# Optimization experiments

Measured on AMD Instinct MI355X. Metric: run time of the kernel, lower is better.

The kernel has to match this reference:

```python
import jax, jax.numpy as jnp
import numpy as np

NUM_HEADS = 12

def setup_inputs() -> dict:
    key = jax.random.key(0)
    k1, k2, k3 = jax.random.split(key, 3)
    dim = 768
    x = jax.random.normal(k1, (1, 64, 64, dim), dtype=jnp.float32)
    qkv_w = jax.random.normal(k2, (3 * dim, dim), dtype=jnp.float32) * (dim ** -0.5)
    qkv_b = jnp.zeros((3 * dim,), dtype=jnp.float32)
    proj_w = jax.random.normal(k3, (dim, dim), dtype=jnp.float32) * (dim ** -0.5)
    proj_b = jnp.zeros((dim,), dtype=jnp.float32)
    return {"x": x, "qkv_w": qkv_w, "qkv_b": qkv_b, "proj_w": proj_w, "proj_b": proj_b}

def reference(x, qkv_w, qkv_b, proj_w, proj_b):
    B, H, W, C = x.shape
    N = H * W
    nh = NUM_HEADS
    # qkv projection: [B,H,W,3C] -> [B,N,3,nh,hd]
    qkv = jnp.einsum('bhwc,dc->bhwd', x, qkv_w) + qkv_b
    qkv = qkv.reshape(B, N, 3, nh, -1)
    q, k, v = qkv[:, :, 0], qkv[:, :, 1], qkv[:, :, 2]  # [B,N,nh,hd]
    q = q.transpose(0, 2, 1, 3)  # [B,nh,N,hd]
    k = k.transpose(0, 2, 1, 3)
    v = v.transpose(0, 2, 1, 3)
    hd = q.shape[-1]
    scale = hd ** -0.5
    scores = jnp.einsum('bhnd,bhmd->bhnm', q, k) * scale  # [B,nh,N,N]
    attn = jax.nn.softmax(scores.astype(jnp.float32), axis=-1).astype(q.dtype)
    attn = jax.lax.stop_gradient(attn)
    out = jnp.einsum('bhnm,bhmd->bhnd', attn, v)  # [B,nh,N,hd]
    out = out.transpose(0, 2, 1, 3).reshape(B, H, W, -1)
    out = jnp.einsum('bhwc,dc->bhwd', out, proj_w) + proj_b
    return out
```

## Files before the change

### kernel.cpp

```cpp
#include <hip/hip_runtime.h>

typedef short short8 __attribute__((ext_vector_type(8)));
typedef short short2v __attribute__((ext_vector_type(2)));
typedef float f32x4 __attribute__((ext_vector_type(4)));
typedef float f32x16 __attribute__((ext_vector_type(16)));
typedef unsigned short ushort4v __attribute__((ext_vector_type(4)));
typedef unsigned int u32;
typedef unsigned int u32x4 __attribute__((ext_vector_type(4)));

__device__ __forceinline__ unsigned short f2b(float f) {
  unsigned u = __builtin_bit_cast(unsigned, f);
  u = u + 0x7FFFu + ((u >> 16) & 1u);
  return (unsigned short)(u >> 16);
}

__device__ __forceinline__ void bar_plain() {
  __builtin_amdgcn_sched_barrier(0);
  asm volatile("" ::: "memory");
  __builtin_amdgcn_s_barrier();
  asm volatile("" ::: "memory");
  __builtin_amdgcn_sched_barrier(0);
}
__device__ __forceinline__ void bar_lgkm() {
  __builtin_amdgcn_sched_barrier(0);
  asm volatile("s_waitcnt lgkmcnt(0)" ::: "memory");
  __builtin_amdgcn_s_barrier();
  asm volatile("" ::: "memory");
  __builtin_amdgcn_sched_barrier(0);
}

__global__ void f2bf3_kernel(const float* __restrict__ a, unsigned short* __restrict__ oa, int na,
                             const float* __restrict__ b, unsigned short* __restrict__ ob, int nb,
                             const float* __restrict__ c, unsigned short* __restrict__ oc, int nc) {
  int i = blockIdx.x * blockDim.x + threadIdx.x;
  const float* in; unsigned short* out;
  if (i < na)           { in = a; out = oa; }
  else if (i < na + nb) { i -= na; in = b; out = ob; }
  else if (i < na + nb + nc) { i -= na + nb; in = c; out = oc; }
  else return;
  float4 v = reinterpret_cast<const float4*>(in)[i];
  ushort4v o;
  o.x = f2b(v.x); o.y = f2b(v.y); o.z = f2b(v.z); o.w = f2b(v.w);
  reinterpret_cast<ushort4v*>(out)[i] = o;
}

__device__ __forceinline__ void store_out(float* C, int idx, float v) { C[idx] = v; }
__device__ __forceinline__ void store_out(short* C, int idx, float v) { C[idx] = (short)f2b(v); }

template <typename OutT>
__global__ __launch_bounds__(256, 2)
void gemm_bt_kernel(const short* __restrict__ A, const short* __restrict__ B,
                    const float* __restrict__ bias, OutT* __restrict__ C,
                    int M, int N, int K, int qcols, float qscale)
{
  __shared__ __align__(16) short lds_a[128][72];
  __shared__ __align__(16) short lds_b[128][72];

  const int tid  = threadIdx.x;
  const int lane = tid & 63;
  const int wave = tid >> 6;
  const int wm   = wave >> 1;
  const int wn   = wave & 1;
  const int r16  = lane & 15;
  const int q4   = lane >> 4;
  const int bm   = blockIdx.x;
  const int bn   = blockIdx.y;

  f32x4 zero = {0.f, 0.f, 0.f, 0.f};
  f32x4 acc[4][4];
#pragma unroll
  for (int i = 0; i < 4; ++i)
#pragma unroll
    for (int j = 0; j < 4; ++j) acc[i][j] = zero;

  const int srow = tid >> 3;
  const int scol = (tid & 7) * 8;
  const short* Ab = A + (bm * 128 + srow) * K + scol;
  const short* Bb = B + (bn * 128 + srow) * K + scol;

  short8 ar[4], br[4];
#pragma unroll
  for (int i = 0; i < 4; ++i) {
    ar[i] = *reinterpret_cast<const short8*>(Ab + i * 32 * K);
    br[i] = *reinterpret_cast<const short8*>(Bb + i * 32 * K);
  }

  const int nk = K >> 6;
  for (int kt = 0; kt < nk; ++kt) {
#pragma unroll
    for (int i = 0; i < 4; ++i) {
      *reinterpret_cast<short8*>(&lds_a[srow + i * 32][scol]) = ar[i];
      *reinterpret_cast<short8*>(&lds_b[srow + i * 32][scol]) = br[i];
    }
    bar_lgkm();
    if (kt + 1 < nk) {
      const short* An = Ab + (kt + 1) * 64;
      const short* Bn = Bb + (kt + 1) * 64;
#pragma unroll
      for (int i = 0; i < 4; ++i) {
        ar[i] = *reinterpret_cast<const short8*>(An + i * 32 * K);
        br[i] = *reinterpret_cast<const short8*>(Bn + i * 32 * K);
      }
    }
#pragma unroll
    for (int kk = 0; kk < 2; ++kk) {
      short8 af[4], bf[4];
#pragma unroll
      for (int mi = 0; mi < 4; ++mi)
        af[mi] = *reinterpret_cast<const short8*>(&lds_a[wm * 64 + mi * 16 + r16][kk * 32 + q4 * 8]);
#pragma unroll
      for (int ni = 0; ni < 4; ++ni)
        bf[ni] = *reinterpret_cast<const short8*>(&lds_b[wn * 64 + ni * 16 + r16][kk * 32 + q4 * 8]);
#pragma unroll
      for (int mi = 0; mi < 4; ++mi)
#pragma unroll
        for (int ni = 0; ni < 4; ++ni)
          acc[mi][ni] = __builtin_amdgcn_mfma_f32_16x16x32_bf16(af[mi], bf[ni], acc[mi][ni], 0, 0, 0);
    }
    bar_plain();
  }

#pragma unroll
  for (int mi = 0; mi < 4; ++mi) {
    const int row0 = bm * 128 + wm * 64 + mi * 16 + q4 * 4;
#pragma unroll
    for (int ni = 0; ni < 4; ++ni) {
      const int col = bn * 128 + wn * 64 + ni * 16 + r16;
      const float bz = bias[col];
      const float sc = (col < qcols) ? qscale : 1.f;
#pragma unroll
      for (int j = 0; j < 4; ++j)
        store_out(C, (row0 + j) * N + col, (acc[mi][ni][j] + bz) * sc);
    }
  }
}

__global__ __launch_bounds__(256, 3)
void attn_kernel(const short* __restrict__ QKV, short* __restrict__ Ao)
{
  constexpr int C3 = 2304;
  __shared__ __align__(16) short k_lds[2][64][64];
  __shared__ __align__(16) short v_lds[2][2][64][64];

  const int tid  = threadIdx.x;
  const int lane = tid & 63;
  const int wave = tid >> 6;
  const int sp   = wave >> 1;
  const int qh   = wave & 1;
  const int l31  = lane & 31;
  const int hi   = lane >> 5;
  const int swz  = l31 & 7;
  const int h    = blockIdx.y;
  const int qt   = blockIdx.x;

  const short* Qp = QKV + h * 64;

  const int qrow = qt * 64 + qh * 32 + l31;
  short8 qf[4];
#pragma unroll
  for (int ks = 0; ks < 4; ++ks)
    qf[ks] = *reinterpret_cast<const short8*>(Qp + qrow * C3 + ks * 16 + hi * 8);

  const int t2 = tid & 127;
  const int kr = t2 >> 3;
  const int kc = t2 & 7;
  const int kswz = 8 * (kc ^ (kr & 7));

  const short* Kt = QKV + 768  + h * 64 + (size_t)(sp * 2048 + kr)     * C3 + kc * 8;
  const short* Vt = QKV + 1536 + h * 64 + (size_t)(sp * 2048 + 2 * kr) * C3 + kc * 8;

  short8 ka[4], va[4];
  auto LOADT = [&]() {
#pragma unroll
    for (int j = 0; j < 4; ++j)
      ka[j] = *reinterpret_cast<const short8*>(Kt + j * 16 * C3);
    va[0] = *reinterpret_cast<const short8*>(Vt);
    va[1] = *reinterpret_cast<const short8*>(Vt + C3);
    va[2] = *reinterpret_cast<const short8*>(Vt + 32 * C3);
    va[3] = *reinterpret_cast<const short8*>(Vt + 33 * C3);
    Kt += 64 * C3; Vt += 64 * C3;
  };

  const int vb3_0 = (2 * kr) >> 3, vko = (2 * kr) & 7;

  short* const vw0 = &v_lds[sp][0][0][0];
  short* const vw1 = &v_lds[sp][1][0][0];
  short* vwr = vw0;
  short* vww = vw1;

  auto WRITET = [&](short* vb) {
#pragma unroll
    for (int j = 0; j < 4; ++j)
      *reinterpret_cast<short8*>(&k_lds[sp][kr + 16 * j][kswz]) = ka[j];
#pragma unroll
    for (int p = 0; p < 2; ++p) {
      const int b3 = vb3_0 + 4 * p;
#pragma unroll
      for (int i = 0; i < 8; ++i) {
        short2v pr; pr.x = va[2 * p][i]; pr.y = va[2 * p + 1][i];
        *reinterpret_cast<short2v*>(vb + (kc * 8 + i) * 64 + 8 * (b3 ^ kc ^ i) + vko) = pr;
      }
    }
  };

  const f32x16 ZEROv = {};
  const short ONE_BF = (short)0x3F80;
  const short8 ONESv = {ONE_BF, ONE_BF, ONE_BF, ONE_BF, ONE_BF, ONE_BF, ONE_BF, ONE_BF};

  f32x16 o0 = {}, o1 = {}, acc_l = {};

  LOADT();
  WRITET(vw0);
  LOADT();
  bar_lgkm();

  for (int kt = 0; kt < 32; ++kt) {
    f32x16 s0, s1;
    {
      const short* kb0 = &k_lds[sp][l31][0];
      const short* kb1 = &k_lds[sp][l31 + 32][0];
      __builtin_amdgcn_s_setprio(1);
#pragma unroll
      for (int ks = 0; ks < 4; ++ks) {
        const int off = 8 * (((ks << 1) | hi) ^ swz);
        short8 kf0 = *reinterpret_cast<const short8*>(kb0 + off);
        short8 kf1 = *reinterpret_cast<const short8*>(kb1 + off);
        s0 = __builtin_amdgcn_mfma_f32_32x32x16_bf16(kf0, qf[ks], ks ? s0 : ZEROv, 0, 0, 0);
        s1 = __builtin_amdgcn_mfma_f32_32x32x16_bf16(kf1, qf[ks], ks ? s1 : ZEROv, 0, 0, 0);
      }
      __builtin_amdgcn_s_setprio(0);
    }
    bar_plain();

    if (kt != 31) {
      WRITET(vww);
      if (kt != 30) LOADT();
    }

#pragma unroll
    for (int i = 0; i < 16; ++i) {
      s0[i] = __builtin_amdgcn_exp2f(s0[i]);
      s1[i] = __builtin_amdgcn_exp2f(s1[i]);
    }

    u32 pkv[4][4];
#pragma unroll
    for (int t = 0; t < 4; ++t) {
      asm("v_cvt_pk_bf16_f32 %0, %1, %2" : "=v"(pkv[0][t]) : "v"(s0[2 * t]),     "v"(s0[2 * t + 1]));
      asm("v_cvt_pk_bf16_f32 %0, %1, %2" : "=v"(pkv[1][t]) : "v"(s0[8 + 2 * t]), "v"(s0[8 + 2 * t + 1]));
      asm("v_cvt_pk_bf16_f32 %0, %1, %2" : "=v"(pkv[2][t]) : "v"(s1[2 * t]),     "v"(s1[2 * t + 1]));
      asm("v_cvt_pk_bf16_f32 %0, %1, %2" : "=v"(pkv[3][t]) : "v"(s1[8 + 2 * t]), "v"(s1[8 + 2 * t + 1]));
    }
#pragma unroll
    for (int ks = 0; ks < 4; ++ks) {
      asm("v_permlane32_swap_b32 %0, %1" : "+v"(pkv[ks][0]), "+v"(pkv[ks][2]));
      asm("v_permlane32_swap_b32 %0, %1" : "+v"(pkv[ks][1]), "+v"(pkv[ks][3]));
    }
    short8 pa[4];
#pragma unroll
    for (int ks = 0; ks < 4; ++ks) {
      u32x4 tmp = {pkv[ks][0], pkv[ks][1], pkv[ks][2], pkv[ks][3]};
      pa[ks] = __builtin_bit_cast(short8, tmp);
    }

#pragma unroll
    for (int ks = 0; ks < 4; ++ks)
      acc_l = __builtin_amdgcn_mfma_f32_32x32x16_bf16(pa[ks], ONESv, acc_l, 0, 0, 0);

    {
      const short* vb0 = vwr + l31 * 64;
      const short* vb1 = vwr + (l31 + 32) * 64;
      const int rsw = (l31 >> 3) ^ (l31 & 7);
      __builtin_amdgcn_s_setprio(1);
#pragma unroll
      for (int ks = 0; ks < 4; ++ks) {
        const int c = ((ks << 1) | hi) ^ rsw;
        short8 vf0 = *reinterpret_cast<const short8*>(vb0 + 8 * c);
        short8 vf1 = *reinterpret_cast<const short8*>(vb1 + 8 * (c ^ 4));
        o0 = __builtin_amdgcn_mfma_f32_32x32x16_bf16(pa[ks], vf0, o0, 0, 0, 0);
        o1 = __builtin_amdgcn_mfma_f32_32x32x16_bf16(pa[ks], vf1, o1, 0, 0, 0);
      }
      __builtin_amdgcn_s_setprio(0);
    }

    { short* t = vwr; vwr = vww; vww = t; }
    bar_lgkm();
  }

  float* o_sh = (float*)&k_lds[0][0][0];
  float* l_sh = (float*)&v_lds[0][0][0][0];

  __syncthreads();
  if (sp == 1) {
#pragma unroll
    for (int r = 0; r < 16; ++r) {
      const int q = (r & 3) + 8 * (r >> 2) + 4 * hi;
      const int row = qh * 32 + q;
      o_sh[row * 64 + l31]      = o0[r];
      o_sh[row * 64 + 32 + l31] = o1[r];
    }
    if (l31 == 0) {
#pragma unroll
      for (int r = 0; r < 16; ++r) {
        const int q = (r & 3) + 8 * (r >> 2) + 4 * hi;
        l_sh[qh * 32 + q] = acc_l[r];
      }
    }
  }
  __syncthreads();
  if (sp == 0) {
#pragma unroll
    for (int r = 0; r < 16; ++r) {
      const int q = (r & 3) + 8 * (r >> 2) + 4 * hi;
      const int row = qh * 32 + q;
      const float lt = 1.f / (acc_l[r] + l_sh[row]);
      const int grow = qt * 64 + row;
      float a0 = (o0[r] + o_sh[row * 64 + l31]) * lt;
      float a1 = (o1[r] + o_sh[row * 64 + 32 + l31]) * lt;
      Ao[grow * 768 + h * 64 + l31]      = (short)f2b(a0);
      Ao[grow * 768 + h * 64 + 32 + l31] = (short)f2b(a1);
    }
  }
}

extern "C" void kernel_launch(void* const* d_in, const int* in_sizes, int n_in,
                              void* d_out, int out_size, void* d_ws, size_t ws_size,
                              hipStream_t stream)
{
  const float* x      = (const float*)d_in[0];
  const float* qkv_w  = (const float*)d_in[1];
  const float* qkv_b  = (const float*)d_in[2];
  const float* proj_w = (const float*)d_in[3];
  const float* proj_b = (const float*)d_in[4];
  float* out = (float*)d_out;

  char* ws = (char*)d_ws;
  short* xb  = (short*)(ws + 0);
  short* wq  = (short*)(ws + 6291456);
  short* wp  = (short*)(ws + 9830400);
  short* qkv = (short*)(ws + 11010048);
  short* ao  = (short*)(ws + 29884416);

  const float sscale = 0.125f * 1.44269504088896340736f;

  f2bf3_kernel<<<5376, 256, 0, stream>>>(x, (unsigned short*)xb, 786432,
                                         qkv_w, (unsigned short*)wq, 442368,
                                         proj_w, (unsigned short*)wp, 147456);

  gemm_bt_kernel<short><<<dim3(32, 18), 256, 0, stream>>>(xb, wq, qkv_b, qkv, 4096, 2304, 768, 768, sscale);
  attn_kernel<<<dim3(64, 12), 256, 0, stream>>>(qkv, ao);
  gemm_bt_kernel<float><<<dim3(32, 6), 256, 0, stream>>>(ao, wp, proj_b, out, 4096, 768, 768, 0, 1.f);
}
```

Baseline: 128.5 us.

## Give each attention wave private K/V LDS tiles and drop block barriers

The attention kernel now gives each wave its own K and V LDS region, which it loads and transposes itself. This replaces the shared double-buffered tiles and the two block-wide barriers per iteration with per-wave lgkmcnt waits. The aim is to remove inter-wave synchronisation stalls, at the cost of duplicate global/L2 loads of K/V across the paired query waves, a larger LDS footprint and more registers per wave. Launch bounds also change: the GEMM goes to 3 blocks per SM and attention to 2.

```diff
diff --git a/kernel.cpp b/kernel.cpp
--- a/kernel.cpp
+++ b/kernel.cpp
@@ -1,7 +1,7 @@
 #include <hip/hip_runtime.h>
 
 typedef short short8 __attribute__((ext_vector_type(8)));
-typedef short short2v __attribute__((ext_vector_type(2)));
+typedef short short4v __attribute__((ext_vector_type(4)));
 typedef float f32x4 __attribute__((ext_vector_type(4)));
 typedef float f32x16 __attribute__((ext_vector_type(16)));
 typedef unsigned short ushort4v __attribute__((ext_vector_type(4)));
@@ -48,7 +48,7 @@
 __device__ __forceinline__ void store_out(short* C, int idx, float v) { C[idx] = (short)f2b(v); }
 
 template <typename OutT>
-__global__ __launch_bounds__(256, 2)
+__global__ __launch_bounds__(256, 3)
 void gemm_bt_kernel(const short* __restrict__ A, const short* __restrict__ B,
                     const float* __restrict__ bias, OutT* __restrict__ C,
                     int M, int N, int K, int qcols, float qscale)
@@ -135,12 +135,11 @@
   }
 }
 
-__global__ __launch_bounds__(256, 3)
+__global__ __launch_bounds__(256, 2)
 void attn_kernel(const short* __restrict__ QKV, short* __restrict__ Ao)
 {
   constexpr int C3 = 2304;
-  __shared__ __align__(16) short k_lds[2][64][64];
-  __shared__ __align__(16) short v_lds[2][2][64][64];
+  __shared__ __align__(16) short kv[4][2][64][64];
 
   const int tid  = threadIdx.x;
   const int lane = tid & 63;
@@ -153,72 +152,74 @@
   const int h    = blockIdx.y;
   const int qt   = blockIdx.x;
 
-  const short* Qp = QKV + h * 64;
-
   const int qrow = qt * 64 + qh * 32 + l31;
   short8 qf[4];
 #pragma unroll
   for (int ks = 0; ks < 4; ++ks)
-    qf[ks] = *reinterpret_cast<const short8*>(Qp + qrow * C3 + ks * 16 + hi * 8);
-
-  const int t2 = tid & 127;
-  const int kr = t2 >> 3;
-  const int kc = t2 & 7;
-  const int kswz = 8 * (kc ^ (kr & 7));
+    qf[ks] = *reinterpret_cast<const short8*>(QKV + h * 64 + qrow * C3 + ks * 16 + hi * 8);
+
+  const int kr = lane >> 3;
+  const int kc = lane & 7;
+  short* const kp = &kv[wave][0][0][0];
+  short* const vp = &kv[wave][1][0][0];
+  const int kswz = 8 * (kc ^ kr);
 
   const short* Kt = QKV + 768  + h * 64 + (size_t)(sp * 2048 + kr)     * C3 + kc * 8;
-  const short* Vt = QKV + 1536 + h * 64 + (size_t)(sp * 2048 + 2 * kr) * C3 + kc * 8;
-
-  short8 ka[4], va[4];
+  const short* Vt = QKV + 1536 + h * 64 + (size_t)(sp * 2048 + 4 * kr) * C3 + kc * 8;
+
+  short8 ka[8], va[8];
   auto LOADT = [&]() {
 #pragma unroll
-    for (int j = 0; j < 4; ++j)
-      ka[j] = *reinterpret_cast<const short8*>(Kt + j * 16 * C3);
-    va[0] = *reinterpret_cast<const short8*>(Vt);
-    va[1] = *reinterpret_cast<const short8*>(Vt + C3);
-    va[2] = *reinterpret_cast<const short8*>(Vt + 32 * C3);
-    va[3] = *reinterpret_cast<const short8*>(Vt + 33 * C3);
+    for (int j = 0; j < 8; ++j)
+      ka[j] = *reinterpret_cast<const short8*>(Kt + j * 8 * C3);
+#pragma unroll
+    for (int j = 0; j < 4; ++j) {
+      va[j]     = *reinterpret_cast<const short8*>(Vt + j * C3);
+      va[4 + j] = *reinterpret_cast<const short8*>(Vt + (32 + j) * C3);
+    }
     Kt += 64 * C3; Vt += 64 * C3;
   };
 
-  const int vb3_0 = (2 * kr) >> 3, vko = (2 * kr) & 7;
-
-  short* const vw0 = &v_lds[sp][0][0][0];
-  short* const vw1 = &v_lds[sp][1][0][0];
-  short* vwr = vw0;
-  short* vww = vw1;
-
-  auto WRITET = [&](short* vb) {
-#pragma unroll
-    for (int j = 0; j < 4; ++j)
-      *reinterpret_cast<short8*>(&k_lds[sp][kr + 16 * j][kswz]) = ka[j];
-#pragma unroll
-    for (int p = 0; p < 2; ++p) {
-      const int b3 = vb3_0 + 4 * p;
-#pragma unroll
-      for (int i = 0; i < 8; ++i) {
-        short2v pr; pr.x = va[2 * p][i]; pr.y = va[2 * p + 1][i];
-        *reinterpret_cast<short2v*>(vb + (kc * 8 + i) * 64 + 8 * (b3 ^ kc ^ i) + vko) = pr;
-      }
+  const int vco = 4 * (kr & 1);
+  const int vch = kr >> 1;
+  auto WRITET = [&]() {
+#pragma unroll
+    for (int j = 0; j < 8; ++j)
+      *reinterpret_cast<short8*>(kp + (kr + 8 * j) * 64 + kswz) = ka[j];
+#pragma unroll
+    for (int i = 0; i < 8; ++i) {
+      short4v p0 = {va[0][i], va[1][i], va[2][i], va[3][i]};
+      short4v p1 = {va[4][i], va[5][i], va[6][i], va[7][i]};
+      const int base = (kc * 8 + i) * 64 + vco;
+      const int c0 = vch ^ kc ^ i;
+      *reinterpret_cast<short4v*>(vp + base + 8 * c0)       = p0;
+      *reinterpret_cast<short4v*>(vp + base + 8 * (c0 ^ 4)) = p1;
     }
   };
 
   const f32x16 ZEROv = {};
   const short ONE_BF = (short)0x3F80;
   const short8 ONESv = {ONE_BF, ONE_BF, ONE_BF, ONE_BF, ONE_BF, ONE_BF, ONE_BF, ONE_BF};
+  const int rsw = (l31 >> 3) ^ (l31 & 7);
 
   f32x16 o0 = {}, o1 = {}, acc_l = {};
 
   LOADT();
-  WRITET(vw0);
-  LOADT();
-  bar_lgkm();
 
   for (int kt = 0; kt < 32; ++kt) {
+    asm volatile("s_waitcnt lgkmcnt(0)" ::: "memory");
+    __builtin_amdgcn_sched_barrier(0);
+
+    WRITET();
+    if (kt != 31) LOADT();
+
+    asm volatile("s_waitcnt lgkmcnt(0)" ::: "memory");
+    __builtin_amdgcn_sched_barrier(0);
+
     f32x16 s0, s1;
     {
-      const short* kb0 = &k_lds[sp][l31][0];
-      const short* kb1 = &k_lds[sp][l31 + 32][0];
+      const short* kb0 = kp + l31 * 64;
+      const short* kb1 = kp + (l31 + 32) * 64;
       __builtin_amdgcn_s_setprio(1);
 #pragma unroll
       for (int ks = 0; ks < 4; ++ks) {
@@ -230,12 +231,6 @@
       }
       __builtin_amdgcn_s_setprio(0);
     }
-    bar_plain();
-
-    if (kt != 31) {
-      WRITET(vww);
-      if (kt != 30) LOADT();
-    }
 
 #pragma unroll
     for (int i = 0; i < 16; ++i) {
@@ -268,9 +263,8 @@
       acc_l = __builtin_amdgcn_mfma_f32_32x32x16_bf16(pa[ks], ONESv, acc_l, 0, 0, 0);
 
     {
-      const short* vb0 = vwr + l31 * 64;
-      const short* vb1 = vwr + (l31 + 32) * 64;
-      const int rsw = (l31 >> 3) ^ (l31 & 7);
+      const short* vb0 = vp + l31 * 64;
+      const short* vb1 = vp + (l31 + 32) * 64;
       __builtin_amdgcn_s_setprio(1);
 #pragma unroll
       for (int ks = 0; ks < 4; ++ks) {
@@ -282,15 +276,13 @@
       }
       __builtin_amdgcn_s_setprio(0);
     }
-
-    { short* t = vwr; vwr = vww; vww = t; }
-    bar_lgkm();
-  }
-
-  float* o_sh = (float*)&k_lds[0][0][0];
-  float* l_sh = (float*)&v_lds[0][0][0][0];
+  }
 
   __syncthreads();
+
+  float* o_sh = (float*)&kv[0][0][0][0];
+  float* l_sh = (float*)&kv[1][0][0][0];
+
   if (sp == 1) {
 #pragma unroll
     for (int r = 0; r < 16; ++r) {
```

Result: slower. 144.6 us (+12.6%).

## Drop split-KV in attention: one 128-thread block walks all keys

Applied to the files above, without the earlier changes.

The attention kernel no longer splits the key range across two wave pairs. Each block now has two waves that loop over all 64 key tiles and normalize directly, which removes the cross-wave reduction through shared memory and its two syncthreads, and halves LDS use per block. The cost is half the waves per block and a sequential loop twice as long, so per-CU latency hiding now depends on fitting more resident blocks. The GEMM launch bound is also raised to three blocks per SIMD, which limits register allocation.

```diff
diff --git a/kernel.cpp b/kernel.cpp
--- a/kernel.cpp
+++ b/kernel.cpp
@@ -48,7 +48,7 @@
 __device__ __forceinline__ void store_out(short* C, int idx, float v) { C[idx] = (short)f2b(v); }
 
 template <typename OutT>
-__global__ __launch_bounds__(256, 2)
+__global__ __launch_bounds__(256, 3)
 void gemm_bt_kernel(const short* __restrict__ A, const short* __restrict__ B,
                     const float* __restrict__ bias, OutT* __restrict__ C,
                     int M, int N, int K, int qcols, float qscale)
@@ -135,39 +135,34 @@
   }
 }
 
-__global__ __launch_bounds__(256, 3)
+__global__ __launch_bounds__(128, 3)
 void attn_kernel(const short* __restrict__ QKV, short* __restrict__ Ao)
 {
   constexpr int C3 = 2304;
-  __shared__ __align__(16) short k_lds[2][64][64];
-  __shared__ __align__(16) short v_lds[2][2][64][64];
+  __shared__ __align__(16) short k_lds[64][64];
+  __shared__ __align__(16) short v_lds[2][64][64];
 
   const int tid  = threadIdx.x;
   const int lane = tid & 63;
   const int wave = tid >> 6;
-  const int sp   = wave >> 1;
-  const int qh   = wave & 1;
   const int l31  = lane & 31;
   const int hi   = lane >> 5;
   const int swz  = l31 & 7;
   const int h    = blockIdx.y;
   const int qt   = blockIdx.x;
 
-  const short* Qp = QKV + h * 64;
-
-  const int qrow = qt * 64 + qh * 32 + l31;
+  const int qrow = qt * 64 + wave * 32 + l31;
   short8 qf[4];
 #pragma unroll
   for (int ks = 0; ks < 4; ++ks)
-    qf[ks] = *reinterpret_cast<const short8*>(Qp + qrow * C3 + ks * 16 + hi * 8);
-
-  const int t2 = tid & 127;
-  const int kr = t2 >> 3;
-  const int kc = t2 & 7;
+    qf[ks] = *reinterpret_cast<const short8*>(QKV + h * 64 + qrow * C3 + ks * 16 + hi * 8);
+
+  const int kr = tid >> 3;
+  const int kc = tid & 7;
   const int kswz = 8 * (kc ^ (kr & 7));
 
-  const short* Kt = QKV + 768  + h * 64 + (size_t)(sp * 2048 + kr)     * C3 + kc * 8;
-  const short* Vt = QKV + 1536 + h * 64 + (size_t)(sp * 2048 + 2 * kr) * C3 + kc * 8;
+  const short* Kt = QKV + 768  + h * 64 + (size_t)kr       * C3 + kc * 8;
+  const short* Vt = QKV + 1536 + h * 64 + (size_t)(2 * kr) * C3 + kc * 8;
 
   short8 ka[4], va[4];
   auto LOADT = [&]() {
@@ -183,15 +178,15 @@
 
   const int vb3_0 = (2 * kr) >> 3, vko = (2 * kr) & 7;
 
-  short* const vw0 = &v_lds[sp][0][0][0];
-  short* const vw1 = &v_lds[sp][1][0][0];
+  short* const vw0 = &v_lds[0][0][0];
+  short* const vw1 = &v_lds[1][0][0];
   short* vwr = vw0;
   short* vww = vw1;
 
   auto WRITET = [&](short* vb) {
 #pragma unroll
     for (int j = 0; j < 4; ++j)
-      *reinterpret_cast<short8*>(&k_lds[sp][kr + 16 * j][kswz]) = ka[j];
+      *reinterpret_cast<short8*>(&k_lds[kr + 16 * j][kswz]) = ka[j];
 #pragma unroll
     for (int p = 0; p < 2; ++p) {
       const int b3 = vb3_0 + 4 * p;
@@ -214,11 +209,11 @@
   LOADT();
   bar_lgkm();
 
-  for (int kt = 0; kt < 32; ++kt) {
+  for (int kt = 0; kt < 64; ++kt) {
     f32x16 s0, s1;
     {
-      const short* kb0 = &k_lds[sp][l31][0];
-      const short* kb1 = &k_lds[sp][l31 + 32][0];
+      const short* kb0 = &k_lds[l31][0];
+      const short* kb1 = &k_lds[l31 + 32][0];
       __builtin_amdgcn_s_setprio(1);
 #pragma unroll
       for (int ks = 0; ks < 4; ++ks) {
@@ -232,9 +227,9 @@
     }
     bar_plain();
 
-    if (kt != 31) {
+    if (kt != 63) {
       WRITET(vww);
-      if (kt != 30) LOADT();
+      if (kt != 62) LOADT();
     }
 
 #pragma unroll
@@ -287,39 +282,13 @@
     bar_lgkm();
   }
 
-  float* o_sh = (float*)&k_lds[0][0][0];
-  float* l_sh = (float*)&v_lds[0][0][0][0];
-
-  __syncthreads();
-  if (sp == 1) {
-#pragma unroll
-    for (int r = 0; r < 16; ++r) {
-      const int q = (r & 3) + 8 * (r >> 2) + 4 * hi;
-      const int row = qh * 32 + q;
-      o_sh[row * 64 + l31]      = o0[r];
-      o_sh[row * 64 + 32 + l31] = o1[r];
-    }
-    if (l31 == 0) {
-#pragma unroll
-      for (int r = 0; r < 16; ++r) {
-        const int q = (r & 3) + 8 * (r >> 2) + 4 * hi;
-        l_sh[qh * 32 + q] = acc_l[r];
-      }
-    }
-  }
-  __syncthreads();
-  if (sp == 0) {
-#pragma unroll
-    for (int r = 0; r < 16; ++r) {
-      const int q = (r & 3) + 8 * (r >> 2) + 4 * hi;
-      const int row = qh * 32 + q;
-      const float lt = 1.f / (acc_l[r] + l_sh[row]);
-      const int grow = qt * 64 + row;
-      float a0 = (o0[r] + o_sh[row * 64 + l31]) * lt;
-      float a1 = (o1[r] + o_sh[row * 64 + 32 + l31]) * lt;
-      Ao[grow * 768 + h * 64 + l31]      = (short)f2b(a0);
-      Ao[grow * 768 + h * 64 + 32 + l31] = (short)f2b(a1);
-    }
+#pragma unroll
+  for (int r = 0; r < 16; ++r) {
+    const int q = (r & 3) + 8 * (r >> 2) + 4 * hi;
+    const float lt = 1.f / acc_l[r];
+    const int grow = qt * 64 + wave * 32 + q;
+    Ao[grow * 768 + h * 64 + l31]      = (short)f2b(o0[r] * lt);
+    Ao[grow * 768 + h * 64 + 32 + l31] = (short)f2b(o1[r] * lt);
   }
 }
 
@@ -348,6 +317,6 @@
                                          proj_w, (unsigned short*)wp, 147456);
 
   gemm_bt_kernel<short><<<dim3(32, 18), 256, 0, stream>>>(xb, wq, qkv_b, qkv, 4096, 2304, 768, 768, sscale);
-  attn_kernel<<<dim3(64, 12), 256, 0, stream>>>(qkv, ao);
+  attn_kernel<<<dim3(64, 12), 128, 0, stream>>>(qkv, ao);
   gemm_bt_kernel<float><<<dim3(32, 6), 256, 0, stream>>>(ao, wp, proj_b, out, 4096, 768, 768, 0, 1.f);
 }
```

Result: slower. 142.0 us (+10.5%).
